# Performance work log

Hardware: AMD Instinct MI355X
Metric: run time of the kernel (lower is better)

Reference implementation:

```python
import jax, jax.numpy as jnp
import numpy as np


def _attention(q, k, v, causal):
    # q,k,v: (B, S, H, D) -> matches flash_attn_func input layout
    B, Sq, H, D = q.shape
    Sk = k.shape[1]
    scale = 1.0 / jnp.sqrt(jnp.asarray(D, dtype=q.dtype))
    # scores: (B, H, Sq, Sk)
    scores = jnp.einsum('bqhd,bkhd->bhqk', q, k) * scale
    if causal:
        # position i attends to j <= i (standard causal mask, Sq == Sk here)
        mask = jnp.tril(jnp.ones((Sq, Sk), dtype=bool))
        scores = jnp.where(mask[None, None], scores, jnp.asarray(-jnp.inf, dtype=scores.dtype))
    probs = jax.nn.softmax(scores, axis=-1)
    out = jnp.einsum('bhqk,bkhd->bqhd', probs, v)
    return out


def setup_inputs() -> dict:
    key = jax.random.key(0)
    kq, kk, kv = jax.random.split(key, 3)
    B, S, H, D = 2, 2048, 16, 128
    q = jax.random.normal(kq, (B, S, H, D), dtype=jnp.float32)
    k = jax.random.normal(kk, (B, S, H, D), dtype=jnp.float32)
    v = jax.random.normal(kv, (B, S, H, D), dtype=jnp.float32)
    return {"q": q, "k": k, "v": v, "causal": 1}


def reference(q, k, v, causal):
    return _attention(q, k, v, bool(causal))
```

## Files before the change

### kernel.cpp

```cpp
#include <hip/hip_runtime.h>

typedef short bf16x8 __attribute__((ext_vector_type(8)));
typedef float f32x16 __attribute__((ext_vector_type(16)));

constexpr int S = 2048;
constexpr int H = 16;
constexpr int D = 128;
constexpr int BM = 128;
constexpr int TILE = 8192;
constexpr int KSTR = 136;


__device__ inline unsigned int pk2(float a, float b) {
    unsigned int ua = __builtin_bit_cast(unsigned int, a);
    unsigned int ub = __builtin_bit_cast(unsigned int, b);
    ua += 0x7fffu + ((ua >> 16) & 1u);
    ub += 0x7fffu + ((ub >> 16) & 1u);
    return (ua >> 16) | (ub & 0xffff0000u);
}

__device__ __forceinline__ void gld16(const unsigned short* g, unsigned short* l) {
    __builtin_amdgcn_global_load_lds(
        (const __attribute__((address_space(1))) unsigned int*)g,
        (__attribute__((address_space(3))) unsigned int*)l, 16, 0, 0);
}

__global__ __launch_bounds__(256) void cvt_kv(const float* __restrict__ K,
                                              const float* __restrict__ V,
                                              unsigned short* __restrict__ Kb,
                                              unsigned short* __restrict__ Vtb) {
    __shared__ unsigned short Vl[64 * KSTR];
    const int tid = threadIdx.x;
    const int t   = blockIdx.x;
    const int bh  = blockIdx.y;
    const int b = bh >> 4, h = bh & 15;
    const size_t base = ((size_t)(b * S + t * 64) * H + h) * D;

    unsigned short* outK = Kb + ((size_t)bh * 32 + t) * TILE;
    #pragma unroll
    for (int u = 0; u < 4; ++u) {
        const int dlin = u * 256 + tid;
        const int grp = dlin >> 7;
        const int s   = dlin & 127;
        const int rho = s >> 4;
        const int c   = (s & 15) ^ rho;
        const float* p = K + base + (size_t)(grp * 8 + rho) * (H * D) + c * 8;
        float4 f0 = *(const float4*)p;
        float4 f1 = *(const float4*)(p + 4);
        unsigned int w[4];
        w[0] = pk2(f0.x, f0.y); w[1] = pk2(f0.z, f0.w);
        w[2] = pk2(f1.x, f1.y); w[3] = pk2(f1.z, f1.w);
        *(uint4*)(outK + dlin * 8) = *(const uint4*)w;
    }

    #pragma unroll
    for (int u = 0; u < 4; ++u) {
        const int cidx = tid + 256 * u;
        const int n    = cidx >> 4;
        const int off  = (cidx & 15) * 8;
        const float* p = V + base + (size_t)n * (H * D) + off;
        float4 f0 = *(const float4*)p;
        float4 f1 = *(const float4*)(p + 4);
        unsigned int w[4];
        w[0] = pk2(f0.x, f0.y); w[1] = pk2(f0.z, f0.w);
        w[2] = pk2(f1.x, f1.y); w[3] = pk2(f1.z, f1.w);
        *(uint4*)&Vl[n * KSTR + off] = *(const uint4*)w;
    }
    __syncthreads();

    const int d  = tid >> 1;
    const int kh = (tid & 1) * 32;
    unsigned short tmp[32];
    #pragma unroll
    for (int m = 0; m < 32; ++m) {
        const int sig = kh + m;
        const int k = (sig & ~12) | ((sig & 4) << 1) | ((sig & 8) >> 1);
        tmp[m] = Vl[k * KSTR + d];
    }
    unsigned short* outV = Vtb + ((size_t)bh * 32 + t) * TILE;
    const int g = d >> 3, rho = d & 7;
    #pragma unroll
    for (int uu = 0; uu < 4; ++uu) {
        const int cc = (kh >> 3) + uu;
        *(uint4*)(outV + g * 512 + (rho * 8 + (cc ^ rho)) * 8) = *(const uint4*)&tmp[uu * 8];
    }
}

__global__ __launch_bounds__(512, 2) void fa_fwd(
    const float* __restrict__ Q,
    const unsigned short* __restrict__ Kb,
    const unsigned short* __restrict__ Vtb,
    const int* __restrict__ causal_p,
    float* __restrict__ Op)
{
    __shared__ unsigned short Kl[2][TILE];
    __shared__ unsigned short Vl[2][TILE];
    __shared__ float mbf[4][64 * 36];
    __shared__ float lbf[4][32];

    const int tid  = threadIdx.x;
    const int w    = tid >> 6;
    const int lane = tid & 63;
    const int ln   = lane & 31;
    const int half = lane >> 5;
    const int qw   = w & 3;
    const int nt   = w >> 2;

    int bh, qp;
    if (gridDim.x == 8 && gridDim.y == 32) {
        const int lid = blockIdx.x + (blockIdx.y << 3);
        const int xcd = lid & 7;
        const int ii  = lid >> 3;
        bh = (xcd << 2) + (ii & 3);
        qp = ii >> 2;
    } else {
        bh = blockIdx.y;
        qp = blockIdx.x;
    }
    const int b = bh >> 4;
    const int h = bh & 15;
    const int causal = *causal_p;
    const float cfold = 0.12751743f;

    const unsigned short* Ksrc = Kb  + (size_t)bh * (32 * TILE);
    const unsigned short* Vsrc = Vtb + (size_t)bh * (32 * TILE);
    const int sgk  = w * 2;
    const int loff = lane * 8;

    const int kb   = (ln >> 3) * 1024 + (ln & 7) * 128;
    const int krho = ln & 7;
    const int vg   = (ln >> 3) * 512;
    const int vrho = ln & 7;

    #pragma unroll 1
    for (int ph = 0; ph < 2; ++ph) {
        const int qblk  = ph ? (15 - qp) : qp;
        const int q0    = qblk * BM;
        const int qrow0 = q0 + qw * 32;
        const int jmax  = causal ? ((q0 + BM - 1) >> 6) : (S / 64 - 1);

        #pragma unroll
        for (int c2 = 0; c2 < 2; ++c2) {
            gld16(Ksrc + (sgk + c2) * 512 + loff, &Kl[0][(sgk + c2) * 512]);
            gld16(Vsrc + (sgk + c2) * 512 + loff, &Vl[0][(sgk + c2) * 512]);
        }

        bf16x8 qf[8];
        {
            const size_t rowoff = ((size_t)(b * S + qrow0 + ln) * H + h) * D;
            #pragma unroll
            for (int c = 0; c < 8; ++c) {
                float4 f0 = *(const float4*)(Q + rowoff + c * 16 + half * 8);
                float4 f1 = *(const float4*)(Q + rowoff + c * 16 + half * 8 + 4);
                unsigned int t[4];
                t[0] = pk2(f0.x * cfold, f0.y * cfold);
                t[1] = pk2(f0.z * cfold, f0.w * cfold);
                t[2] = pk2(f1.x * cfold, f1.y * cfold);
                t[3] = pk2(f1.z * cfold, f1.w * cfold);
                qf[c] = *(const bf16x8*)t;
            }
        }

        f32x16 o[4];
        #pragma unroll
        for (int dt = 0; dt < 4; ++dt)
            #pragma unroll
            for (int r = 0; r < 16; ++r) o[dt][r] = 0.0f;
        float l = 0.0f;

        asm volatile("s_waitcnt vmcnt(0)" ::: "memory");
        __builtin_amdgcn_s_barrier();

        int cur = 0;
        #pragma unroll 1
        for (int j = 0; j <= jmax; ++j) {
            if (j < jmax) {
                const unsigned short* ks = Ksrc + (size_t)(j + 1) * TILE;
                const unsigned short* vs = Vsrc + (size_t)(j + 1) * TILE;
                #pragma unroll
                for (int c2 = 0; c2 < 2; ++c2) {
                    gld16(ks + (sgk + c2) * 512 + loff, &Kl[cur ^ 1][(sgk + c2) * 512]);
                    gld16(vs + (sgk + c2) * 512 + loff, &Vl[cur ^ 1][(sgk + c2) * 512]);
                }
            }

            const bool wact = (!causal) || (j * 64 + nt * 32 <= qrow0 + 31);
            if (wact) {
                f32x16 sacc;
                #pragma unroll
                for (int r = 0; r < 16; ++r) sacc[r] = 0.0f;
                const unsigned short* kl = &Kl[cur][nt * 4096 + kb];
                __builtin_amdgcn_s_setprio(1);
                #pragma unroll
                for (int c = 0; c < 8; ++c) {
                    uint4 raw = *(const uint4*)(kl + (((2 * c + half) ^ krho) << 3));
                    bf16x8 kf = *(const bf16x8*)&raw;
                    sacc = __builtin_amdgcn_mfma_f32_32x32x16_bf16(kf, qf[c], sacc, 0, 0, 0);
                }
                __builtin_amdgcn_s_setprio(0);

                float p[16];
                const int thr  = qrow0 + ln - j * 64;
                const bool full = (!causal) || (j * 64 + 63 <= qrow0);
                #pragma unroll
                for (int r = 0; r < 16; ++r) {
                    float e = __builtin_amdgcn_exp2f(sacc[r]);
                    if (!full) {
                        const int kl_ = nt * 32 + (r & 3) + 8 * (r >> 2) + 4 * half;
                        if (kl_ > thr) e = 0.0f;
                    }
                    l += e;
                    p[r] = e;
                }

                __builtin_amdgcn_s_setprio(1);
                #pragma unroll
                for (int win2 = 0; win2 < 2; ++win2) {
                    unsigned int pw[4];
                    #pragma unroll
                    for (int d2 = 0; d2 < 4; ++d2)
                        pw[d2] = pk2(p[win2 * 8 + 2 * d2], p[win2 * 8 + 2 * d2 + 1]);
                    bf16x8 pf = *(const bf16x8*)pw;
                    const int cc = (nt * 2 + win2) * 2 + half;
                    const int voff = ((vrho * 8) + (cc ^ vrho)) << 3;
                    #pragma unroll
                    for (int dt = 0; dt < 4; ++dt) {
                        uint4 raw = *(const uint4*)(&Vl[cur][dt * 2048 + vg + voff]);
                        bf16x8 vf = *(const bf16x8*)&raw;
                        o[dt] = __builtin_amdgcn_mfma_f32_32x32x16_bf16(vf, pf, o[dt], 0, 0, 0);
                    }
                }
                __builtin_amdgcn_s_setprio(0);
            }

            asm volatile("s_waitcnt vmcnt(0)" ::: "memory");
            __builtin_amdgcn_s_barrier();
            cur ^= 1;
        }

        const float lp = l + __shfl_xor(l, 32);
        float* mb = mbf[qw];
        if (w >= 4) {
            #pragma unroll
            for (int dt = 0; dt < 2; ++dt)
                #pragma unroll
                for (int r = 0; r < 16; ++r)
                    mb[lane * 36 + dt * 16 + r] = o[dt][r];
            if (half == 0) lbf[qw][ln] = lp;
        }
        __syncthreads();
        float ltot = 1.0f;
        if (w < 4) {
            #pragma unroll
            for (int dt = 0; dt < 2; ++dt)
                #pragma unroll
                for (int r = 0; r < 16; ++r)
                    o[dt][r] += mb[lane * 36 + dt * 16 + r];
            ltot = lp + lbf[qw][ln];
        }
        __syncthreads();
        if (w >= 4) {
            #pragma unroll
            for (int dt = 2; dt < 4; ++dt)
                #pragma unroll
                for (int r = 0; r < 16; ++r)
                    mb[lane * 36 + (dt - 2) * 16 + r] = o[dt][r];
        }
        __syncthreads();
        if (w < 4) {
            #pragma unroll
            for (int dt = 2; dt < 4; ++dt)
                #pragma unroll
                for (int r = 0; r < 16; ++r)
                    o[dt][r] += mb[lane * 36 + (dt - 2) * 16 + r];

            const float inv = 1.0f / ltot;
            float* op = Op + ((size_t)(b * S + qrow0 + ln) * H + h) * D;
            #pragma unroll
            for (int dt = 0; dt < 4; ++dt)
                #pragma unroll
                for (int rq = 0; rq < 4; ++rq) {
                    float4 st;
                    st.x = o[dt][rq * 4 + 0] * inv;
                    st.y = o[dt][rq * 4 + 1] * inv;
                    st.z = o[dt][rq * 4 + 2] * inv;
                    st.w = o[dt][rq * 4 + 3] * inv;
                    *(float4*)(op + dt * 32 + 8 * rq + 4 * half) = st;
                }
        }
        __syncthreads();
    }
}

extern "C" void kernel_launch(void* const* d_in, const int* in_sizes, int n_in,
                              void* d_out, int out_size, void* d_ws, size_t ws_size,
                              hipStream_t stream) {
    const int B = in_sizes[0] / (S * H * D);
    unsigned short* Kb  = (unsigned short*)d_ws;
    unsigned short* Vtb = Kb + (size_t)B * S * H * D;

    cvt_kv<<<dim3(S / 64, B * H), 256, 0, stream>>>(
        (const float*)d_in[1], (const float*)d_in[2], Kb, Vtb);
    fa_fwd<<<dim3(8, B * H), 512, 0, stream>>>(
        (const float*)d_in[0], Kb, Vtb, (const int*)d_in[3], (float*)d_out);
}
```

Measured before the change: 191.6 us.

## Software-pipeline QK^T one tile ahead with triple-buffered K/V in LDS

The attention loop now triple-buffers the K/V tiles in LDS and prefetches two tiles ahead. It computes the next tile's QK^T MFMAs before the current tile's exp and PV MFMAs, so score computation overlaps with the softmax and value work. The reduction scratch buffer is aliased into the K buffer with a padded stride of 33 to save LDS, and the row-sum accumulation is split into two partial sums. The conversion kernel stages transposed V in LDS so global writes are coalesced. The cost is more LDS per block (three 32KB buffer pairs), which may cut occupancy below two blocks per CU, and extra registers for the second score accumulator.

Result: no change. 193.4 us (+0.9%).

```diff
diff --git a/kernel.cpp b/kernel.cpp
--- a/kernel.cpp
+++ b/kernel.cpp
@@ -9,6 +9,7 @@
 constexpr int BM = 128;
 constexpr int TILE = 8192;
 constexpr int KSTR = 136;
+constexpr int MST = 33;
 
 
 __device__ inline unsigned int pk2(float a, float b) {
@@ -29,7 +30,8 @@
                                               const float* __restrict__ V,
                                               unsigned short* __restrict__ Kb,
                                               unsigned short* __restrict__ Vtb) {
-    __shared__ unsigned short Vl[64 * KSTR];
+    __shared__ unsigned short Vst[64 * KSTR];
+    __shared__ unsigned short Vout[TILE];
     const int tid = threadIdx.x;
     const int t   = blockIdx.x;
     const int bh  = blockIdx.y;
@@ -64,7 +66,7 @@
         unsigned int w[4];
         w[0] = pk2(f0.x, f0.y); w[1] = pk2(f0.z, f0.w);
         w[2] = pk2(f1.x, f1.y); w[3] = pk2(f1.z, f1.w);
-        *(uint4*)&Vl[n * KSTR + off] = *(const uint4*)w;
+        *(uint4*)&Vst[n * KSTR + off] = *(const uint4*)w;
     }
     __syncthreads();
 
@@ -75,14 +77,21 @@
     for (int m = 0; m < 32; ++m) {
         const int sig = kh + m;
         const int k = (sig & ~12) | ((sig & 4) << 1) | ((sig & 8) >> 1);
-        tmp[m] = Vl[k * KSTR + d];
-    }
-    unsigned short* outV = Vtb + ((size_t)bh * 32 + t) * TILE;
+        tmp[m] = Vst[k * KSTR + d];
+    }
     const int g = d >> 3, rho = d & 7;
     #pragma unroll
     for (int uu = 0; uu < 4; ++uu) {
         const int cc = (kh >> 3) + uu;
-        *(uint4*)(outV + g * 512 + (rho * 8 + (cc ^ rho)) * 8) = *(const uint4*)&tmp[uu * 8];
+        *(uint4*)&Vout[g * 512 + (rho * 8 + (cc ^ rho)) * 8] = *(const uint4*)&tmp[uu * 8];
+    }
+    __syncthreads();
+
+    unsigned short* outV = Vtb + ((size_t)bh * 32 + t) * TILE;
+    #pragma unroll
+    for (int u = 0; u < 4; ++u) {
+        const int dlin = u * 256 + tid;
+        *(uint4*)(outV + dlin * 8) = *(const uint4*)&Vout[dlin * 8];
     }
 }
 
@@ -93,9 +102,8 @@
     const int* __restrict__ causal_p,
     float* __restrict__ Op)
 {
-    __shared__ unsigned short Kl[2][TILE];
-    __shared__ unsigned short Vl[2][TILE];
-    __shared__ float mbf[4][64 * 36];
+    __shared__ unsigned short Kl[3][TILE];
+    __shared__ unsigned short Vl[3][TILE];
     __shared__ float lbf[4][32];
 
     const int tid  = threadIdx.x;
@@ -144,6 +152,11 @@
             gld16(Ksrc + (sgk + c2) * 512 + loff, &Kl[0][(sgk + c2) * 512]);
             gld16(Vsrc + (sgk + c2) * 512 + loff, &Vl[0][(sgk + c2) * 512]);
         }
+        #pragma unroll
+        for (int c2 = 0; c2 < 2; ++c2) {
+            gld16(Ksrc + TILE + (sgk + c2) * 512 + loff, &Kl[1][(sgk + c2) * 512]);
+            gld16(Vsrc + TILE + (sgk + c2) * 512 + loff, &Vl[1][(sgk + c2) * 512]);
+        }
 
         bf16x8 qf[8];
         {
@@ -171,47 +184,70 @@
         asm volatile("s_waitcnt vmcnt(0)" ::: "memory");
         __builtin_amdgcn_s_barrier();
 
+        f32x16 sacc_c, sacc_n;
+        if ((!causal) || (nt * 32 <= qrow0 + 31)) {
+            #pragma unroll
+            for (int r = 0; r < 16; ++r) sacc_c[r] = 0.0f;
+            const unsigned short* kl = &Kl[0][nt * 4096 + kb];
+            #pragma unroll
+            for (int c = 0; c < 8; ++c) {
+                uint4 raw = *(const uint4*)(kl + (((2 * c + half) ^ krho) << 3));
+                bf16x8 kf = *(const bf16x8*)&raw;
+                sacc_c = __builtin_amdgcn_mfma_f32_32x32x16_bf16(kf, qf[c], sacc_c, 0, 0, 0);
+            }
+        }
+
         int cur = 0;
         #pragma unroll 1
         for (int j = 0; j <= jmax; ++j) {
-            if (j < jmax) {
-                const unsigned short* ks = Ksrc + (size_t)(j + 1) * TILE;
-                const unsigned short* vs = Vsrc + (size_t)(j + 1) * TILE;
+            if (j > 0) {
+                asm volatile("s_waitcnt vmcnt(0)" ::: "memory");
+                __builtin_amdgcn_s_barrier();
+            }
+            if (j + 2 <= jmax) {
+                int nb = cur + 2; if (nb >= 3) nb -= 3;
+                const unsigned short* ks = Ksrc + (size_t)(j + 2) * TILE;
+                const unsigned short* vs = Vsrc + (size_t)(j + 2) * TILE;
                 #pragma unroll
                 for (int c2 = 0; c2 < 2; ++c2) {
-                    gld16(ks + (sgk + c2) * 512 + loff, &Kl[cur ^ 1][(sgk + c2) * 512]);
-                    gld16(vs + (sgk + c2) * 512 + loff, &Vl[cur ^ 1][(sgk + c2) * 512]);
-                }
-            }
-
-            const bool wact = (!causal) || (j * 64 + nt * 32 <= qrow0 + 31);
-            if (wact) {
-                f32x16 sacc;
-                #pragma unroll
-                for (int r = 0; r < 16; ++r) sacc[r] = 0.0f;
-                const unsigned short* kl = &Kl[cur][nt * 4096 + kb];
+                    gld16(ks + (sgk + c2) * 512 + loff, &Kl[nb][(sgk + c2) * 512]);
+                    gld16(vs + (sgk + c2) * 512 + loff, &Vl[nb][(sgk + c2) * 512]);
+                }
+            }
+
+            const bool actj = (!causal) || (j * 64 + nt * 32 <= qrow0 + 31);
+
+            if (j < jmax && ((!causal) || ((j + 1) * 64 + nt * 32 <= qrow0 + 31))) {
+                int nx = cur + 1; if (nx >= 3) nx -= 3;
+                #pragma unroll
+                for (int r = 0; r < 16; ++r) sacc_n[r] = 0.0f;
+                const unsigned short* kl = &Kl[nx][nt * 4096 + kb];
                 __builtin_amdgcn_s_setprio(1);
                 #pragma unroll
                 for (int c = 0; c < 8; ++c) {
                     uint4 raw = *(const uint4*)(kl + (((2 * c + half) ^ krho) << 3));
                     bf16x8 kf = *(const bf16x8*)&raw;
-                    sacc = __builtin_amdgcn_mfma_f32_32x32x16_bf16(kf, qf[c], sacc, 0, 0, 0);
+                    sacc_n = __builtin_amdgcn_mfma_f32_32x32x16_bf16(kf, qf[c], sacc_n, 0, 0, 0);
                 }
                 __builtin_amdgcn_s_setprio(0);
-
+            }
+
+            if (actj) {
                 float p[16];
                 const int thr  = qrow0 + ln - j * 64;
                 const bool full = (!causal) || (j * 64 + 63 <= qrow0);
+                float l0 = 0.0f, l1 = 0.0f;
                 #pragma unroll
                 for (int r = 0; r < 16; ++r) {
-                    float e = __builtin_amdgcn_exp2f(sacc[r]);
+                    float e = __builtin_amdgcn_exp2f(sacc_c[r]);
                     if (!full) {
                         const int kl_ = nt * 32 + (r & 3) + 8 * (r >> 2) + 4 * half;
                         if (kl_ > thr) e = 0.0f;
                     }
-                    l += e;
+                    if (r & 1) l1 += e; else l0 += e;
                     p[r] = e;
                 }
+                l += l0 + l1;
 
                 __builtin_amdgcn_s_setprio(1);
                 #pragma unroll
@@ -233,19 +269,20 @@
                 __builtin_amdgcn_s_setprio(0);
             }
 
-            asm volatile("s_waitcnt vmcnt(0)" ::: "memory");
-            __builtin_amdgcn_s_barrier();
-            cur ^= 1;
-        }
+            sacc_c = sacc_n;
+            cur += 1; if (cur >= 3) cur -= 3;
+        }
+
+        __syncthreads();
 
         const float lp = l + __shfl_xor(l, 32);
-        float* mb = mbf[qw];
+        float* mb = reinterpret_cast<float*>(&Kl[0][0]) + qw * (64 * MST);
         if (w >= 4) {
             #pragma unroll
             for (int dt = 0; dt < 2; ++dt)
                 #pragma unroll
                 for (int r = 0; r < 16; ++r)
-                    mb[lane * 36 + dt * 16 + r] = o[dt][r];
+                    mb[lane * MST + dt * 16 + r] = o[dt][r];
             if (half == 0) lbf[qw][ln] = lp;
         }
         __syncthreads();
@@ -255,7 +292,7 @@
             for (int dt = 0; dt < 2; ++dt)
                 #pragma unroll
                 for (int r = 0; r < 16; ++r)
-                    o[dt][r] += mb[lane * 36 + dt * 16 + r];
+                    o[dt][r] += mb[lane * MST + dt * 16 + r];
             ltot = lp + lbf[qw][ln];
         }
         __syncthreads();
@@ -264,7 +301,7 @@
             for (int dt = 2; dt < 4; ++dt)
                 #pragma unroll
                 for (int r = 0; r < 16; ++r)
-                    mb[lane * 36 + (dt - 2) * 16 + r] = o[dt][r];
+                    mb[lane * MST + (dt - 2) * 16 + r] = o[dt][r];
         }
         __syncthreads();
         if (w < 4) {
@@ -272,7 +309,7 @@
             for (int dt = 2; dt < 4; ++dt)
                 #pragma unroll
                 for (int r = 0; r < 16; ++r)
-                    o[dt][r] += mb[lane * 36 + (dt - 2) * 16 + r];
+                    o[dt][r] += mb[lane * MST + (dt - 2) * 16 + r];
 
             const float inv = 1.0f / ltot;
             float* op = Op + ((size_t)(b * S + qrow0 + ln) * H + h) * D;
```

## Load K/V fragments directly from global into registers, drop LDS double buffer

Applied to the files above, without the earlier changes.

Rewrites the conversion kernel so K and V tiles are emitted in an MFMA-fragment-ordered layout. The attention kernel can then load each wave's K and V fragments straight from global memory into registers, prefetching the next tile during compute. This removes the LDS staging buffers and the per-iteration waitcnt plus block barrier, and it also reduces the reduction buffer padding stride. In exchange it raises register pressure (16 uint4 prefetch registers) and relies on cache hits, since the 4 query waves sharing a key half now each fetch the same K/V data from global separately.

New measurement: 187.2 us. 1.02x faster.

```diff
diff --git a/kernel.cpp b/kernel.cpp
--- a/kernel.cpp
+++ b/kernel.cpp
@@ -9,6 +9,7 @@
 constexpr int BM = 128;
 constexpr int TILE = 8192;
 constexpr int KSTR = 136;
+constexpr int MST  = 33;
 
 
 __device__ inline unsigned int pk2(float a, float b) {
@@ -19,54 +20,48 @@
     return (ua >> 16) | (ub & 0xffff0000u);
 }
 
-__device__ __forceinline__ void gld16(const unsigned short* g, unsigned short* l) {
-    __builtin_amdgcn_global_load_lds(
-        (const __attribute__((address_space(1))) unsigned int*)g,
-        (__attribute__((address_space(3))) unsigned int*)l, 16, 0, 0);
-}
-
 __global__ __launch_bounds__(256) void cvt_kv(const float* __restrict__ K,
                                               const float* __restrict__ V,
                                               unsigned short* __restrict__ Kb,
                                               unsigned short* __restrict__ Vtb) {
-    __shared__ unsigned short Vl[64 * KSTR];
+    __shared__ unsigned short Kst[64 * KSTR];
+    __shared__ unsigned short Vst[64 * KSTR];
+    __shared__ unsigned short Vout[TILE];
     const int tid = threadIdx.x;
     const int t   = blockIdx.x;
     const int bh  = blockIdx.y;
     const int b = bh >> 4, h = bh & 15;
     const size_t base = ((size_t)(b * S + t * 64) * H + h) * D;
 
-    unsigned short* outK = Kb + ((size_t)bh * 32 + t) * TILE;
     #pragma unroll
     for (int u = 0; u < 4; ++u) {
-        const int dlin = u * 256 + tid;
-        const int grp = dlin >> 7;
-        const int s   = dlin & 127;
-        const int rho = s >> 4;
-        const int c   = (s & 15) ^ rho;
-        const float* p = K + base + (size_t)(grp * 8 + rho) * (H * D) + c * 8;
-        float4 f0 = *(const float4*)p;
-        float4 f1 = *(const float4*)(p + 4);
+        const int c   = tid + 256 * u;
+        const int n   = c >> 4;
+        const int off = (c & 15) * 8;
+        const float* pk = K + base + (size_t)n * (H * D) + off;
+        float4 f0 = *(const float4*)pk;
+        float4 f1 = *(const float4*)(pk + 4);
         unsigned int w[4];
         w[0] = pk2(f0.x, f0.y); w[1] = pk2(f0.z, f0.w);
         w[2] = pk2(f1.x, f1.y); w[3] = pk2(f1.z, f1.w);
-        *(uint4*)(outK + dlin * 8) = *(const uint4*)w;
-    }
-
-    #pragma unroll
-    for (int u = 0; u < 4; ++u) {
-        const int cidx = tid + 256 * u;
-        const int n    = cidx >> 4;
-        const int off  = (cidx & 15) * 8;
-        const float* p = V + base + (size_t)n * (H * D) + off;
-        float4 f0 = *(const float4*)p;
-        float4 f1 = *(const float4*)(p + 4);
-        unsigned int w[4];
+        *(uint4*)&Kst[n * KSTR + off] = *(const uint4*)w;
+        const float* pv = V + base + (size_t)n * (H * D) + off;
+        f0 = *(const float4*)pv;
+        f1 = *(const float4*)(pv + 4);
         w[0] = pk2(f0.x, f0.y); w[1] = pk2(f0.z, f0.w);
         w[2] = pk2(f1.x, f1.y); w[3] = pk2(f1.z, f1.w);
-        *(uint4*)&Vl[n * KSTR + off] = *(const uint4*)w;
+        *(uint4*)&Vst[n * KSTR + off] = *(const uint4*)w;
     }
     __syncthreads();
+
+    unsigned short* outK = Kb + ((size_t)bh * 32 + t) * TILE;
+    #pragma unroll
+    for (int u = 0; u < 4; ++u) {
+        const int s = u * 256 + tid;
+        const int chunk = s >> 6;
+        const int row   = s & 63;
+        *(uint4*)(outK + s * 8) = *(const uint4*)&Kst[row * KSTR + chunk * 8];
+    }
 
     const int d  = tid >> 1;
     const int kh = (tid & 1) * 32;
@@ -75,14 +70,19 @@
     for (int m = 0; m < 32; ++m) {
         const int sig = kh + m;
         const int k = (sig & ~12) | ((sig & 4) << 1) | ((sig & 8) >> 1);
-        tmp[m] = Vl[k * KSTR + d];
-    }
-    unsigned short* outV = Vtb + ((size_t)bh * 32 + t) * TILE;
-    const int g = d >> 3, rho = d & 7;
+        tmp[m] = Vst[k * KSTR + d];
+    }
     #pragma unroll
     for (int uu = 0; uu < 4; ++uu) {
         const int cc = (kh >> 3) + uu;
-        *(uint4*)(outV + g * 512 + (rho * 8 + (cc ^ rho)) * 8) = *(const uint4*)&tmp[uu * 8];
+        *(uint4*)&Vout[(cc * 128 + d) * 8] = *(const uint4*)&tmp[uu * 8];
+    }
+    __syncthreads();
+    unsigned short* outV = Vtb + ((size_t)bh * 32 + t) * TILE;
+    #pragma unroll
+    for (int u = 0; u < 4; ++u) {
+        const int s = u * 256 + tid;
+        *(uint4*)(outV + s * 8) = *(const uint4*)&Vout[s * 8];
     }
 }
 
@@ -93,9 +93,7 @@
     const int* __restrict__ causal_p,
     float* __restrict__ Op)
 {
-    __shared__ unsigned short Kl[2][TILE];
-    __shared__ unsigned short Vl[2][TILE];
-    __shared__ float mbf[4][64 * 36];
+    __shared__ float mbf[4][64 * MST];
     __shared__ float lbf[4][32];
 
     const int tid  = threadIdx.x;
@@ -122,15 +120,10 @@
     const int causal = *causal_p;
     const float cfold = 0.12751743f;
 
-    const unsigned short* Ksrc = Kb  + (size_t)bh * (32 * TILE);
-    const unsigned short* Vsrc = Vtb + (size_t)bh * (32 * TILE);
-    const int sgk  = w * 2;
-    const int loff = lane * 8;
-
-    const int kb   = (ln >> 3) * 1024 + (ln & 7) * 128;
-    const int krho = ln & 7;
-    const int vg   = (ln >> 3) * 512;
-    const int vrho = ln & 7;
+    const unsigned short* Kc = Kb  + (size_t)bh * (32 * TILE);
+    const unsigned short* Vc = Vtb + (size_t)bh * (32 * TILE);
+    const int koff  = half * 512 + nt * 256 + ln * 8;
+    const int vkoff = (nt * 4 + half) * 1024 + ln * 8;
 
     #pragma unroll 1
     for (int ph = 0; ph < 2; ++ph) {
@@ -138,12 +131,6 @@
         const int q0    = qblk * BM;
         const int qrow0 = q0 + qw * 32;
         const int jmax  = causal ? ((q0 + BM - 1) >> 6) : (S / 64 - 1);
-
-        #pragma unroll
-        for (int c2 = 0; c2 < 2; ++c2) {
-            gld16(Ksrc + (sgk + c2) * 512 + loff, &Kl[0][(sgk + c2) * 512]);
-            gld16(Vsrc + (sgk + c2) * 512 + loff, &Vl[0][(sgk + c2) * 512]);
-        }
 
         bf16x8 qf[8];
         {
@@ -166,78 +153,83 @@
         for (int dt = 0; dt < 4; ++dt)
             #pragma unroll
             for (int r = 0; r < 16; ++r) o[dt][r] = 0.0f;
-        float l = 0.0f;
-
-        asm volatile("s_waitcnt vmcnt(0)" ::: "memory");
-        __builtin_amdgcn_s_barrier();
-
-        int cur = 0;
+        float l0 = 0.0f, l1 = 0.0f;
+
+        uint4 kr[8], vr[8];
+        if ((!causal) || (nt * 32 <= qrow0 + 31)) {
+            #pragma unroll
+            for (int c = 0; c < 8; ++c)
+                kr[c] = *(const uint4*)(Kc + c * 1024 + koff);
+            #pragma unroll
+            for (int i = 0; i < 8; ++i)
+                vr[i] = *(const uint4*)(Vc + (i >> 2) * 2048 + (i & 3) * 256 + vkoff);
+        }
+
         #pragma unroll 1
         for (int j = 0; j <= jmax; ++j) {
-            if (j < jmax) {
-                const unsigned short* ks = Ksrc + (size_t)(j + 1) * TILE;
-                const unsigned short* vs = Vsrc + (size_t)(j + 1) * TILE;
-                #pragma unroll
-                for (int c2 = 0; c2 < 2; ++c2) {
-                    gld16(ks + (sgk + c2) * 512 + loff, &Kl[cur ^ 1][(sgk + c2) * 512]);
-                    gld16(vs + (sgk + c2) * 512 + loff, &Vl[cur ^ 1][(sgk + c2) * 512]);
-                }
-            }
-
-            const bool wact = (!causal) || (j * 64 + nt * 32 <= qrow0 + 31);
-            if (wact) {
-                f32x16 sacc;
+            const bool aj = (!causal) || (j * 64 + nt * 32 <= qrow0 + 31);
+            const bool an = (j < jmax) &&
+                            ((!causal) || ((j + 1) * 64 + nt * 32 <= qrow0 + 31));
+
+            f32x16 sacc;
+            if (aj) {
                 #pragma unroll
                 for (int r = 0; r < 16; ++r) sacc[r] = 0.0f;
-                const unsigned short* kl = &Kl[cur][nt * 4096 + kb];
                 __builtin_amdgcn_s_setprio(1);
                 #pragma unroll
                 for (int c = 0; c < 8; ++c) {
-                    uint4 raw = *(const uint4*)(kl + (((2 * c + half) ^ krho) << 3));
-                    bf16x8 kf = *(const bf16x8*)&raw;
+                    bf16x8 kf = *(const bf16x8*)&kr[c];
                     sacc = __builtin_amdgcn_mfma_f32_32x32x16_bf16(kf, qf[c], sacc, 0, 0, 0);
                 }
                 __builtin_amdgcn_s_setprio(0);
-
-                float p[16];
+            }
+            if (an) {
+                const unsigned short* kt = Kc + (size_t)(j + 1) * TILE;
+                #pragma unroll
+                for (int c = 0; c < 8; ++c)
+                    kr[c] = *(const uint4*)(kt + c * 1024 + koff);
+            }
+
+            if (aj) {
                 const int thr  = qrow0 + ln - j * 64;
                 const bool full = (!causal) || (j * 64 + 63 <= qrow0);
-                #pragma unroll
-                for (int r = 0; r < 16; ++r) {
-                    float e = __builtin_amdgcn_exp2f(sacc[r]);
-                    if (!full) {
-                        const int kl_ = nt * 32 + (r & 3) + 8 * (r >> 2) + 4 * half;
-                        if (kl_ > thr) e = 0.0f;
-                    }
-                    l += e;
-                    p[r] = e;
-                }
-
                 __builtin_amdgcn_s_setprio(1);
                 #pragma unroll
                 for (int win2 = 0; win2 < 2; ++win2) {
                     unsigned int pw[4];
                     #pragma unroll
-                    for (int d2 = 0; d2 < 4; ++d2)
-                        pw[d2] = pk2(p[win2 * 8 + 2 * d2], p[win2 * 8 + 2 * d2 + 1]);
+                    for (int d2 = 0; d2 < 4; ++d2) {
+                        const int r0 = win2 * 8 + 2 * d2;
+                        const int r1 = r0 + 1;
+                        float e0 = __builtin_amdgcn_exp2f(sacc[r0]);
+                        float e1 = __builtin_amdgcn_exp2f(sacc[r1]);
+                        if (!full) {
+                            const int k0 = nt * 32 + (r0 & 3) + 8 * (r0 >> 2) + 4 * half;
+                            const int k1 = nt * 32 + (r1 & 3) + 8 * (r1 >> 2) + 4 * half;
+                            if (k0 > thr) e0 = 0.0f;
+                            if (k1 > thr) e1 = 0.0f;
+                        }
+                        l0 += e0; l1 += e1;
+                        pw[d2] = pk2(e0, e1);
+                    }
                     bf16x8 pf = *(const bf16x8*)pw;
-                    const int cc = (nt * 2 + win2) * 2 + half;
-                    const int voff = ((vrho * 8) + (cc ^ vrho)) << 3;
                     #pragma unroll
                     for (int dt = 0; dt < 4; ++dt) {
-                        uint4 raw = *(const uint4*)(&Vl[cur][dt * 2048 + vg + voff]);
-                        bf16x8 vf = *(const bf16x8*)&raw;
+                        bf16x8 vf = *(const bf16x8*)&vr[win2 * 4 + dt];
                         o[dt] = __builtin_amdgcn_mfma_f32_32x32x16_bf16(vf, pf, o[dt], 0, 0, 0);
                     }
                 }
                 __builtin_amdgcn_s_setprio(0);
             }
-
-            asm volatile("s_waitcnt vmcnt(0)" ::: "memory");
-            __builtin_amdgcn_s_barrier();
-            cur ^= 1;
-        }
-
+            if (an) {
+                const unsigned short* vt = Vc + (size_t)(j + 1) * TILE;
+                #pragma unroll
+                for (int i = 0; i < 8; ++i)
+                    vr[i] = *(const uint4*)(vt + (i >> 2) * 2048 + (i & 3) * 256 + vkoff);
+            }
+        }
+
+        const float l = l0 + l1;
         const float lp = l + __shfl_xor(l, 32);
         float* mb = mbf[qw];
         if (w >= 4) {
@@ -245,7 +237,7 @@
             for (int dt = 0; dt < 2; ++dt)
                 #pragma unroll
                 for (int r = 0; r < 16; ++r)
-                    mb[lane * 36 + dt * 16 + r] = o[dt][r];
+                    mb[lane * MST + dt * 16 + r] = o[dt][r];
             if (half == 0) lbf[qw][ln] = lp;
         }
         __syncthreads();
@@ -255,7 +247,7 @@
             for (int dt = 0; dt < 2; ++dt)
                 #pragma unroll
                 for (int r = 0; r < 16; ++r)
-                    o[dt][r] += mb[lane * 36 + dt * 16 + r];
+                    o[dt][r] += mb[lane * MST + dt * 16 + r];
             ltot = lp + lbf[qw][ln];
         }
         __syncthreads();
@@ -264,7 +256,7 @@
             for (int dt = 2; dt < 4; ++dt)
                 #pragma unroll
                 for (int r = 0; r < 16; ++r)
-                    mb[lane * 36 + (dt - 2) * 16 + r] = o[dt][r];
+                    mb[lane * MST + (dt - 2) * 16 + r] = o[dt][r];
         }
         __syncthreads();
         if (w < 4) {
@@ -272,7 +264,7 @@
             for (int dt = 2; dt < 4; ++dt)
                 #pragma unroll
                 for (int r = 0; r < 16; ++r)
-                    o[dt][r] += mb[lane * 36 + (dt - 2) * 16 + r];
+                    o[dt][r] += mb[lane * MST + (dt - 2) * 16 + r];
 
             const float inv = 1.0f / ltot;
             float* op = Op + ((size_t)(b * S + qrow0 + ln) * H + h) * D;
```
